# Kernel optimization log

Hardware: AMD Instinct MI355X
Metric: run time of the kernel (lower is better)

The kernel has to match this reference:

```python
import jax, jax.numpy as jnp
import numpy as np

K_NEIGHBORS = 3  # init kwarg k_neighbors


def setup_inputs() -> dict:
    key = jax.random.key(0)
    k1, k2 = jax.random.split(key)
    q = jax.random.normal(k1, (75, 640, 21, 21), dtype=jnp.float32)
    S = jax.random.normal(k2, (5, 640, 21, 21), dtype=jnp.float32)
    return {"q": q, "S": S, "qAV_num": 1, "SAV_num": 1, "shot_num": 1}


def reference(q, S, qAV_num, SAV_num, shot_num):
    B, C = q.shape[0], q.shape[1]
    # [B, HW, C], L2-normalize each local descriptor over channels
    qd = q.reshape(B, C, -1).transpose(0, 2, 1)
    qd = qd / jnp.linalg.norm(qd, axis=2, keepdims=True)

    N = S.shape[0]
    sd = S.reshape(N, C, -1).transpose(0, 2, 1)  # [N, HW, C]
    sd = sd / jnp.linalg.norm(sd, axis=2, keepdims=True)
    HW = sd.shape[1]
    M = SAV_num * shot_num * HW
    # group support images into classes: [ncls, C, M]
    sup = sd.reshape(-1, M, C).transpose(0, 2, 1)
    ncls = sup.shape[0]

    # cosine similarity: [B, ncls, HW, M]
    ip = jnp.einsum('bqc,ncm->bnqm', qd, sup)
    # split AV groups: [B//qAV, qAV, ncls, HW, M]
    ip = ip.reshape(B // qAV_num, qAV_num, ncls, HW, M)
    # top-k along the query-descriptor (HW) axis (torch dim=-2)
    topk = jax.lax.top_k(jnp.swapaxes(ip, -1, -2), K_NEIGHBORS)[0]  # [..., M, k]
    img2class = topk.sum(axis=(-1, -2))  # [B', qAV, ncls]
    # geometric mean over the AV axis (dim=1)
    sim = jnp.exp(jnp.mean(jnp.log(img2class), axis=1))  # [B', ncls]
    return sim
```

## Files before the change

### kernel.cpp

```cpp
#include <hip/hip_runtime.h>
#include <hip/hip_bf16.h>


#define B_IMGS 75
#define N_CLS  5
#define C_DIM  640
#define HW     441
#define HWP    448
#define NKT    20
#define NRB    28
#define CHUNK  512
#define TPAD   66

typedef __attribute__((ext_vector_type(8))) short  short8;
typedef __attribute__((ext_vector_type(4))) float  float4v;

__device__ __forceinline__ void ins3(float& t0, float& t1, float& t2, float v) {
    float m  = fminf(t0, v);
    t0 = fmaxf(t0, v);
    float m2 = fminf(t1, m);
    t1 = fmaxf(t1, m);
    t2 = fmaxf(t2, m2);
}

__device__ __forceinline__ void glds16(const __hip_bfloat16* g, __hip_bfloat16* l) {
    __builtin_amdgcn_global_load_lds(
        (const __attribute__((address_space(1))) unsigned int*)g,
        (__attribute__((address_space(3))) unsigned int*)l, 16, 0, 0);
}

__global__ __launch_bounds__(256)
void norm_kernel(const float* __restrict__ q, const float* __restrict__ S,
                 float* __restrict__ invn) {
    __shared__ float part[4][64];
    int bid = blockIdx.x;
    int img = bid / 7;
    int h0  = bid % 7;
    const float* src = (img < B_IMGS)
        ? q + (size_t)img * C_DIM * HW
        : S + (size_t)(img - B_IMGS) * C_DIM * HW;
    int t  = threadIdx.x;
    int hl = t & 63;
    int p  = t >> 6;
    int hw = h0 * 64 + hl;
    int hwc = (hw < HW) ? hw : (HW - 1);

    float ss = 0.f;
    for (int c0 = p * 160; c0 < (p + 1) * 160; c0 += 16) {
        float v[16];
#pragma unroll
        for (int j = 0; j < 16; ++j) v[j] = src[(size_t)(c0 + j) * HW + hwc];
#pragma unroll
        for (int j = 0; j < 16; ++j) ss += v[j] * v[j];
    }
    part[p][hl] = ss;
    __syncthreads();
    if (t < 64) {
        float tot = part[0][t] + part[1][t] + part[2][t] + part[3][t];
        invn[img * HWP + h0 * 64 + t] = (h0 * 64 + t < HW) ? rsqrtf(tot) : 0.f;
    }
}

__global__ __launch_bounds__(256)
void pack_kernel(const float* __restrict__ q, const float* __restrict__ S,
                 const float* __restrict__ invn,
                 __hip_bfloat16* __restrict__ qn2, __hip_bfloat16* __restrict__ sn2) {
    __shared__ __hip_bfloat16 tile[128][TPAD];
    int bid = blockIdx.x;
    int img = bid / 35;
    int rem = bid % 35;
    int h0  = rem / 5;
    int ktg = rem % 5;
    const float* src; __hip_bfloat16* dst;
    if (img < B_IMGS) {
        src = q + (size_t)img * C_DIM * HW;
        dst = qn2 + (size_t)img * NRB * NKT * CHUNK;
    } else {
        src = S + (size_t)(img - B_IMGS) * C_DIM * HW;
        dst = sn2 + (size_t)(img - B_IMGS) * NRB * NKT * CHUNK;
    }
    int t  = threadIdx.x;
    int hl = t & 63;
    int p  = t >> 6;
    int hw = h0 * 64 + hl;
    int hwc = (hw < HW) ? hw : (HW - 1);
    float iv = invn[img * HWP + h0 * 64 + hl];

    for (int c0 = p * 32; c0 < p * 32 + 32; c0 += 8) {
        float v[8];
#pragma unroll
        for (int j = 0; j < 8; ++j)
            v[j] = src[(size_t)(ktg * 128 + c0 + j) * HW + hwc];
#pragma unroll
        for (int j = 0; j < 8; ++j)
            tile[c0 + j][hl] = __float2bfloat16(v[j] * iv);
    }
    __syncthreads();

    int tl  = t & 63;
    int row = tl & 15;
    int oct = tl >> 4;
    int rb  = h0 * 4 + p;
    for (int ktl = 0; ktl < 4; ++ktl) {
        int kt = ktg * 4 + ktl;
        short8 v;
#pragma unroll
        for (int j = 0; j < 8; ++j) {
            __hip_bfloat16 hv = tile[ktl * 32 + oct * 8 + j][p * 16 + row];
            v[j] = *(short*)&hv;
        }
        *(short8*)(dst + ((size_t)rb * NKT + kt) * CHUNK + tl * 8) = v;
    }
}

__global__ __launch_bounds__(256, 2)
void gemm_top3_kernel(const __hip_bfloat16* __restrict__ qn2,
                      const __hip_bfloat16* __restrict__ sn2,
                      float* __restrict__ out) {
    __shared__ __hip_bfloat16 sbuf[64 * CHUNK];
    __shared__ float mrg[4][64][3];

    int id  = blockIdx.x;
    int xcd = id & 7;
    int j8  = id >> 3;
    int b   = (j8 / 35) * 8 + xcd;
    if (b >= B_IMGS) return;
    int inner = j8 % 35;
    int n  = inner / 7;
    int mt = inner % 7;

    int tid  = threadIdx.x;
    int w    = tid >> 6;
    int lane = tid & 63;
    int c16  = lane & 15;
    int quad = lane >> 4;
    int frag = lane * 8;

    const __hip_bfloat16* qA = qn2 + (size_t)b * NRB * NKT * CHUNK;
    const __hip_bfloat16* qB = sn2 + ((size_t)n * NRB + mt * 4) * NKT * CHUNK;

    float4v acc[7][4];
#pragma unroll
    for (int r = 0; r < 7; ++r)
#pragma unroll
        for (int j = 0; j < 4; ++j)
            acc[r][j] = (float4v){0.f, 0.f, 0.f, 0.f};

    for (int s = 0; s < 10; ++s) {
        __syncthreads();
#pragma unroll
        for (int i = 0; i < 16; ++i) {
            int cid = w * 16 + i;
            const __hip_bfloat16* g;
            if (cid < 56) {
                int rb = cid >> 1;
                g = qA + ((size_t)rb * NKT + 2 * s + (cid & 1)) * CHUNK;
            } else {
                int jb = (cid - 56) >> 1;
                g = qB + ((size_t)jb * NKT + 2 * s + (cid & 1)) * CHUNK;
            }
            glds16(g + lane * 8, sbuf + cid * CHUNK + lane * 8);
        }
        __syncthreads();

#pragma unroll
        for (int kk = 0; kk < 2; ++kk) {
            short8 a[7], bfr[4];
#pragma unroll
            for (int r = 0; r < 7; ++r)
                a[r] = *(const short8*)(sbuf + ((r * 4 + w) * 2 + kk) * CHUNK + frag);
#pragma unroll
            for (int j = 0; j < 4; ++j)
                bfr[j] = *(const short8*)(sbuf + (56 + j * 2 + kk) * CHUNK + frag);
#pragma unroll
            for (int r = 0; r < 7; ++r)
#pragma unroll
                for (int j = 0; j < 4; ++j)
                    acc[r][j] = __builtin_amdgcn_mfma_f32_16x16x32_bf16(
                        a[r], bfr[j], acc[r][j], 0, 0, 0);
        }
    }

    float T0[4], T1[4], T2[4];
#pragma unroll
    for (int j = 0; j < 4; ++j) { T0[j] = -1e30f; T1[j] = -1e30f; T2[j] = -1e30f; }
#pragma unroll
    for (int r = 0; r < 7; ++r)
#pragma unroll
        for (int j = 0; j < 4; ++j)
#pragma unroll
            for (int g = 0; g < 4; ++g) {
                int row = r * 64 + w * 16 + quad * 4 + g;
                float v = (row < HW) ? acc[r][j][g] : -1e30f;
                ins3(T0[j], T1[j], T2[j], v);
            }

#pragma unroll
    for (int j = 0; j < 4; ++j) {
#pragma unroll
        for (int d = 16; d <= 32; d <<= 1) {
            float o0 = __shfl_xor(T0[j], d, 64);
            float o1 = __shfl_xor(T1[j], d, 64);
            float o2 = __shfl_xor(T2[j], d, 64);
            ins3(T0[j], T1[j], T2[j], o0);
            ins3(T0[j], T1[j], T2[j], o1);
            ins3(T0[j], T1[j], T2[j], o2);
        }
    }

    if (quad == 0) {
#pragma unroll
        for (int j = 0; j < 4; ++j) {
            mrg[w][j * 16 + c16][0] = T0[j];
            mrg[w][j * 16 + c16][1] = T1[j];
            mrg[w][j * 16 + c16][2] = T2[j];
        }
    }
    __syncthreads();
    if (tid < 64) {
        int col = tid;
        float t0 = mrg[0][col][0], t1 = mrg[0][col][1], t2 = mrg[0][col][2];
#pragma unroll
        for (int ww = 1; ww < 4; ++ww) {
            ins3(t0, t1, t2, mrg[ww][col][0]);
            ins3(t0, t1, t2, mrg[ww][col][1]);
            ins3(t0, t1, t2, mrg[ww][col][2]);
        }
        float s = (mt * 64 + col < HW) ? (t0 + t1 + t2) : 0.f;
#pragma unroll
        for (int d = 32; d >= 1; d >>= 1) s += __shfl_xor(s, d, 64);
        if (tid == 0) atomicAdd(&out[b * N_CLS + n], s);
    }
}

extern "C" void kernel_launch(void* const* d_in, const int* in_sizes, int n_in,
                              void* d_out, int out_size, void* d_ws, size_t ws_size,
                              hipStream_t stream) {
    const float* q = (const float*)d_in[0];
    const float* S = (const float*)d_in[1];
    float* out = (float*)d_out;

    char* ws = (char*)d_ws;
    size_t off = 0;
    __hip_bfloat16* qn2 = (__hip_bfloat16*)(ws + off);
    off += (size_t)B_IMGS * NRB * NKT * CHUNK * 2;  off = (off + 255) & ~(size_t)255;
    __hip_bfloat16* sn2 = (__hip_bfloat16*)(ws + off);
    off += (size_t)N_CLS * NRB * NKT * CHUNK * 2;   off = (off + 255) & ~(size_t)255;
    float* invn = (float*)(ws + off);

    hipMemsetAsync(d_out, 0, (size_t)out_size * sizeof(float), stream);

    norm_kernel<<<dim3(80 * 7), dim3(256), 0, stream>>>(q, S, invn);
    pack_kernel<<<dim3(80 * 7 * 5), dim3(256), 0, stream>>>(q, S, invn, qn2, sn2);
    gemm_top3_kernel<<<dim3(8 * 350), dim3(256), 0, stream>>>(qn2, sn2, out);
}
```

Baseline: 284.0 us.

## Double-buffer LDS tiles in GEMM top-3 kernel to overlap loads with MFMA

Restructures the K loop of the fused GEMM/top-3 kernel so it walks 20 single k-tiles instead of 10 pairs. Each tile is staged into one of two shared-memory buffers while the other is being consumed, with explicit vmcnt waits and raw barriers in place of full __syncthreads. Fragments are loaded to registers before a second barrier, so the next prefetch can safely overwrite the buffer. It also raises wave priority around the MFMA block. The goal is to hide global-to-LDS load latency behind matrix math, at the cost of more barriers per unit of work and hand-tuned waitcnt correctness.

```diff
diff --git a/kernel.cpp b/kernel.cpp
--- a/kernel.cpp
+++ b/kernel.cpp
@@ -117,7 +117,7 @@
 void gemm_top3_kernel(const __hip_bfloat16* __restrict__ qn2,
                       const __hip_bfloat16* __restrict__ sn2,
                       float* __restrict__ out) {
-    __shared__ __hip_bfloat16 sbuf[64 * CHUNK];
+    __shared__ __hip_bfloat16 sbuf[2][32 * CHUNK];
     __shared__ float mrg[4][64][3];
 
     int id  = blockIdx.x;
@@ -146,39 +146,46 @@
         for (int j = 0; j < 4; ++j)
             acc[r][j] = (float4v){0.f, 0.f, 0.f, 0.f};
 
-    for (int s = 0; s < 10; ++s) {
-        __syncthreads();
-#pragma unroll
-        for (int i = 0; i < 16; ++i) {
-            int cid = w * 16 + i;
-            const __hip_bfloat16* g;
-            if (cid < 56) {
-                int rb = cid >> 1;
-                g = qA + ((size_t)rb * NKT + 2 * s + (cid & 1)) * CHUNK;
-            } else {
-                int jb = (cid - 56) >> 1;
-                g = qB + ((size_t)jb * NKT + 2 * s + (cid & 1)) * CHUNK;
-            }
-            glds16(g + lane * 8, sbuf + cid * CHUNK + lane * 8);
-        }
-        __syncthreads();
-
-#pragma unroll
-        for (int kk = 0; kk < 2; ++kk) {
-            short8 a[7], bfr[4];
-#pragma unroll
-            for (int r = 0; r < 7; ++r)
-                a[r] = *(const short8*)(sbuf + ((r * 4 + w) * 2 + kk) * CHUNK + frag);
+    auto stage = [&](int kt, int pb) {
+#pragma unroll
+        for (int i = 0; i < 8; ++i) {
+            int cid = w * 8 + i;
+            const __hip_bfloat16* g = (cid < 28)
+                ? qA + ((size_t)cid * NKT + kt) * CHUNK
+                : qB + ((size_t)(cid - 28) * NKT + kt) * CHUNK;
+            glds16(g + lane * 8, &sbuf[pb][cid * CHUNK + lane * 8]);
+        }
+    };
+
+    stage(0, 0);
+    for (int kt = 0; kt < NKT; ++kt) {
+        int p = kt & 1;
+        if (kt + 1 < NKT) stage(kt + 1, p ^ 1);
+        if (kt + 1 < NKT)
+            asm volatile("s_waitcnt vmcnt(8)" ::: "memory");
+        else
+            asm volatile("s_waitcnt vmcnt(0)" ::: "memory");
+        __builtin_amdgcn_s_barrier();
+
+        short8 a[7], bfr[4];
+#pragma unroll
+        for (int r = 0; r < 7; ++r)
+            a[r] = *(const short8*)(&sbuf[p][(r * 4 + w) * CHUNK + frag]);
+#pragma unroll
+        for (int j = 0; j < 4; ++j)
+            bfr[j] = *(const short8*)(&sbuf[p][(28 + j) * CHUNK + frag]);
+        asm volatile("s_waitcnt lgkmcnt(0)" ::: "memory");
+        __builtin_amdgcn_sched_barrier(0);
+        __builtin_amdgcn_s_barrier();
+
+        __builtin_amdgcn_s_setprio(1);
+#pragma unroll
+        for (int r = 0; r < 7; ++r)
 #pragma unroll
             for (int j = 0; j < 4; ++j)
-                bfr[j] = *(const short8*)(sbuf + (56 + j * 2 + kk) * CHUNK + frag);
-#pragma unroll
-            for (int r = 0; r < 7; ++r)
-#pragma unroll
-                for (int j = 0; j < 4; ++j)
-                    acc[r][j] = __builtin_amdgcn_mfma_f32_16x16x32_bf16(
-                        a[r], bfr[j], acc[r][j], 0, 0, 0);
-        }
+                acc[r][j] = __builtin_amdgcn_mfma_f32_16x16x32_bf16(
+                    a[r], bfr[j], acc[r][j], 0, 0, 0);
+        __builtin_amdgcn_s_setprio(0);
     }
 
     float T0[4], T1[4], T2[4];
```

Result: slower. 297.7 us (+4.8%).
